# Performance work log

Hardware: AMD Instinct MI355X
Metric: run time of the kernel (lower is better)

Reference implementation:

```python
import jax, jax.numpy as jnp
import numpy as np

N_MELS = 80
HID = 512
N_CLS = 64
DT = 0.1  # LTC integration step (reconstructed DREAMCell constant)


def setup_inputs() -> dict:
    key = jax.random.key(0)
    ks = jax.random.split(key, 16)
    s = lambda fan: 1.0 / np.sqrt(fan)
    inp = {
        "feats": jax.random.normal(ks[0], (32, 2048, N_MELS), dtype=jnp.float32),
        # cell 0: input_dim = N_MELS
        "C0": jax.random.normal(ks[1], (N_MELS, HID), jnp.float32) * s(HID),
        "B0": jax.random.normal(ks[2], (HID, N_MELS), jnp.float32) * s(N_MELS),
        "W0": jax.random.normal(ks[3], (HID, N_MELS), jnp.float32) * s(N_MELS),
        "tau0_0": jnp.float32(1.0),
        "gamma0": jnp.float32(0.25),
        "ltc_tau0": jax.random.normal(ks[4], (HID,), jnp.float32) * 0.1,
        # cell 1: input_dim = HID (receives base_eff of cell 0)
        "C1": jax.random.normal(ks[5], (HID, HID), jnp.float32) * s(HID),
        "B1": jax.random.normal(ks[6], (HID, HID), jnp.float32) * s(HID),
        "W1": jax.random.normal(ks[7], (HID, HID), jnp.float32) * s(HID),
        "tau0_1": jnp.float32(1.0),
        "gamma1": jnp.float32(0.25),
        "ltc_tau1": jax.random.normal(ks[8], (HID,), jnp.float32) * 0.1,
        # head: Linear(2*HID, N_CLS)
        "head_w": jax.random.normal(ks[9], (N_CLS, 2 * HID), jnp.float32) * s(2 * HID),
        "head_b": jnp.zeros((N_CLS,), jnp.float32),
    }
    return inp


def _step_cell(params, h, x_t):
    C, Bm, W, tau0, gamma, ltc_tau = params
    # x_t: (B, D_in), h: (B, HID)
    x_scale = jnp.clip(jnp.linalg.norm(x_t, axis=-1, keepdims=True), 1e-6, None)  # (B,1)
    x_norm = jnp.clip(x_t / x_scale, -1.0, 1.0)
    hd = jax.lax.stop_gradient(h)
    error = x_t - jnp.tanh(hd @ C.T) * x_scale  # (B, D_in)
    rel_err = jnp.minimum(
        jnp.linalg.norm(error, axis=-1) / jax.lax.stop_gradient(x_scale[:, 0]), 4.0
    )  # (B,)
    surprise = jax.nn.sigmoid((rel_err - tau0) / gamma)  # (B,)
    base_eff = x_norm @ Bm.T  # (B, HID)
    err_eff = error @ W.T  # (B, HID)
    input_h = hd * 0.2 + base_eff * 0.6 + err_eff * surprise[:, None] * 0.2
    # LTC update (reconstructed): surprise-modulated liquid time constant
    tau_eff = 1.0 + jax.nn.softplus(ltc_tau)  # (HID,)
    alpha = (DT / tau_eff) * (1.0 + surprise[:, None])
    h_new = h + alpha * (jnp.tanh(input_h) - h)
    return h_new, base_eff


def _forward(feats, cell_params, head_w, head_b):
    B = feats.shape[0]
    h0 = tuple(jnp.zeros((B, HID), feats.dtype) for _ in cell_params)

    def body(hs, x_t):
        x = x_t
        new_hs = []
        for p, h in zip(cell_params, hs):
            h, be = _step_cell(p, h, x)
            new_hs.append(h)
            x = be
        out_t = jnp.concatenate([new_hs[-1], x], axis=-1)  # (B, 2*HID)
        return tuple(new_hs), out_t

    xs = jnp.swapaxes(feats, 0, 1)  # (T, B, N_MELS)
    _, outs = jax.lax.scan(body, h0, xs)  # (T, B, 2*HID)
    outs = jnp.swapaxes(outs, 0, 1)  # (B, T, 2*HID)
    return outs @ head_w.T + head_b  # (B, T, N_CLS)


def reference(feats, C0, B0, W0, tau0_0, gamma0, ltc_tau0,
              C1, B1, W1, tau0_1, gamma1, ltc_tau1, head_w, head_b):
    cell_params = [
        (C0, B0, W0, tau0_0, gamma0, ltc_tau0),
        (C1, B1, W1, tau0_1, gamma1, ltc_tau1),
    ]
    return _forward(feats, cell_params, head_w, head_b)
```

## Files before the change

### kernel.cpp

```cpp
#include <hip/hip_runtime.h>
#include <hip/hip_fp16.h>
#include <math.h>

#define BATCHN 32
#define SEQT   2048
#define NMELS  80
#define HIDN   512
#define NCLSN  64
#define BTROWS (BATCHN*SEQT)

typedef unsigned long long u64;
typedef _Float16 __attribute__((ext_vector_type(2))) h2v;

__device__ inline float wave_sum(float v) {
  #pragma unroll
  for (int o = 32; o > 0; o >>= 1) v += __shfl_xor(v, o, 64);
  return v;
}
__device__ inline float ftanh(float x) {
  float ax = fabsf(x);
  float e = __expf(2.0f*ax);
  float t = 1.0f - 2.0f/(e + 1.0f);
  return copysignf(t, x);
}
__device__ inline unsigned pkh2(float a, float b) {
  __half2 h = __floats2half2_rn(a, b);
  return *(unsigned*)&h;
}
__device__ inline float fdot2(unsigned a, unsigned b, float c) {
#if __has_builtin(__builtin_amdgcn_fdot2)
  union { unsigned u; h2v v; } ua, ub; ua.u = a; ub.u = b;
  return __builtin_amdgcn_fdot2(ua.v, ub.v, c, false);
#else
  union { unsigned u; __half2 h; } ua, ub; ua.u = a; ub.u = b;
  float2 fa = __half22float2(ua.h), fb = __half22float2(ub.h);
  return c + fa.x*fb.x + fa.y*fb.y;
#endif
}
__device__ inline u64 pk64(float v, unsigned ep) {
  union { float f; unsigned u; } c; c.f = v;
  return ((u64)ep << 32) | (u64)c.u;
}
__device__ inline float lo32f(u64 q) {
  union { unsigned u; float f; } c; c.u = (unsigned)q; return c.f;
}
__device__ inline void st64(u64* p, u64 v) {
  __hip_atomic_store(p, v, __ATOMIC_RELAXED, __HIP_MEMORY_SCOPE_AGENT);
}
__device__ inline u64 ld64(const u64* p) {
  return __hip_atomic_load(p, __ATOMIC_RELAXED, __HIP_MEMORY_SCOPE_AGENT);
}

__global__ __launch_bounds__(256) void rownorm_kernel(
    const float* __restrict__ X, float* __restrict__ xs, int M, int K)
{
  int wave = threadIdx.x >> 6, lane = threadIdx.x & 63;
  int m = blockIdx.x*4 + wave;
  if (m >= M) return;
  const float* row = X + (size_t)m*K;
  float acc = 0.f;
  for (int k = lane; k < K; k += 64) { float v = row[k]; acc += v*v; }
  acc = wave_sum(acc);
  if (lane == 0) xs[m] = fmaxf(sqrtf(acc), 1e-6f);
}

__global__ __launch_bounds__(256) void initout_kernel(
    float* __restrict__ out, const float* __restrict__ head_b)
{
  int i4 = blockIdx.x*256 + threadIdx.x;
  float4 v = ((const float4*)head_b)[i4 & 15];
  ((float4*)out)[i4] = v;
}

__global__ __launch_bounds__(256, 1) void recur_kernel(
    const float* __restrict__ feats,
    const float* __restrict__ B0,
    const float* __restrict__ C1, const float* __restrict__ B1,
    const float* __restrict__ W1,
    const float* __restrict__ ltc,
    const float* __restrict__ tau0p, const float* __restrict__ gammap,
    const float* __restrict__ head_w,
    const float* __restrict__ xs0v,
    float* __restrict__ out,
    u64* __restrict__ PG)
{
  const int wg = blockIdx.x;
  const int x = wg & 7, s = (wg >> 3) & 7, qq = wg >> 6;
  const int b = x*4 + qq;
  const int row0 = s*64;
  const int tid = threadIdx.x;
  const int r = tid >> 2, kc = tid & 3;
  const int wid = tid >> 6, lane = tid & 63;

  __shared__ u64      b0t_s[20*512];
  __shared__ float    whh_s[64*68];
  __shared__ float    whb_s[64*68];
  __shared__ unsigned er2_s[256];
  __shared__ unsigned bo2_s[256];
  __shared__ unsigned ft2_s[40];
  __shared__ float    h_s[64];
  __shared__ float    bv_s[64];
  __shared__ float    a0_s[64];
  __shared__ float    red_s[4], red0_s[4];

  unsigned c1a[32], c1b[32];
  unsigned w1h[64];
  unsigned b1h[64];
  {
    const float* srcA = C1 + (size_t)tid*512 + row0;
    const float* srcB = C1 + (size_t)(tid+256)*512 + row0;
    #pragma unroll
    for (int j = 0; j < 16; j++) {
      float4 va = *(const float4*)(srcA + 4*j);
      float4 vb = *(const float4*)(srcB + 4*j);
      c1a[2*j] = pkh2(va.x, va.y); c1a[2*j+1] = pkh2(va.z, va.w);
      c1b[2*j] = pkh2(vb.x, vb.y); c1b[2*j+1] = pkh2(vb.z, vb.w);
    }
  }
  {
    const float* src = W1 + (size_t)(row0 + r)*512 + kc*64;
    #pragma unroll
    for (int u4 = 0; u4 < 16; u4++) {
      float4 va = *(const float4*)(src + 4*u4);
      float4 vb = *(const float4*)(src + 256 + 4*u4);
      w1h[4*u4+0] = pkh2(va.x, vb.x); w1h[4*u4+1] = pkh2(va.y, vb.y);
      w1h[4*u4+2] = pkh2(va.z, vb.z); w1h[4*u4+3] = pkh2(va.w, vb.w);
    }
  }
  {
    const float* src = B1 + (size_t)(row0 + r)*512 + kc*64;
    #pragma unroll
    for (int u4 = 0; u4 < 16; u4++) {
      float4 va = *(const float4*)(src + 4*u4);
      float4 vb = *(const float4*)(src + 256 + 4*u4);
      b1h[4*u4+0] = pkh2(va.x, vb.x); b1h[4*u4+1] = pkh2(va.y, vb.y);
      b1h[4*u4+2] = pkh2(va.z, vb.z); b1h[4*u4+3] = pkh2(va.w, vb.w);
    }
  }
  for (int i = tid; i < 20*512; i += 256) {
    int k4 = i >> 9, row = i & 511;
    float4 v = *(const float4*)(B0 + (size_t)row*80 + 4*k4);
    b0t_s[i] = (u64)pkh2(v.x, v.y) | ((u64)pkh2(v.z, v.w) << 32);
  }
  for (int i = tid; i < 4096; i += 256) {
    int c = i >> 6, j = i & 63;
    whh_s[c*68+j] = head_w[(size_t)c*1024 + row0 + j];
    whb_s[c*68+j] = head_w[(size_t)c*1024 + 512 + row0 + j];
  }
  if (tid < 64) {
    float xv = ltc[row0 + tid];
    float spl = (xv > 20.f) ? xv : log1pf(__expf(xv));
    a0_s[tid] = 0.1f / (1.0f + spl);
    h_s[tid] = 0.f;
  }
  const float tau0v = *tau0p, gmv = *gammap;
  __syncthreads();

  float bev0 = 0.f, bev1 = 0.f, xsc = 1.f, rxs_c = 1.f;
  float ftn = 0.f, rxs0n = 1.f;

  auto shadow = [&]() {
    float fo = __shfl_xor(ftn, 1, 64);
    if (tid < 80 && (tid & 1) == 0) ft2_s[tid >> 1] = pkh2(ftn, fo);
    __syncthreads();
    float a0v = 0.f, a1v = 0.f;
    #pragma unroll
    for (int k4 = 0; k4 < 20; k4++) {
      unsigned fA = ft2_s[2*k4], fB = ft2_s[2*k4+1];
      u64 qa = b0t_s[k4*512 + tid];
      u64 qb = b0t_s[k4*512 + tid + 256];
      a0v = fdot2((unsigned)qa, fA, a0v); a0v = fdot2((unsigned)(qa >> 32), fB, a0v);
      a1v = fdot2((unsigned)qb, fA, a1v); a1v = fdot2((unsigned)(qb >> 32), fB, a1v);
    }
    const float b0n = a0v * rxs0n, b1n = a1v * rxs0n;
    float sq = wave_sum(b0n*b0n + b1n*b1n);
    if (lane == 0) red0_s[wid] = sq;
    __syncthreads();
    const float xsq = red0_s[0]+red0_s[1]+red0_s[2]+red0_s[3];
    const float xs1n = fmaxf(sqrtf(xsq), 1e-6f);
    const float rx1n = 1.0f / xs1n;
    bo2_s[tid] = pkh2(b0n*rx1n, b1n*rx1n);
    __syncthreads();
    float pb = 0.f;
    #pragma unroll
    for (int u4 = 0; u4 < 16; u4++) {
      uint4 ov = *(const uint4*)(bo2_s + kc*64 + 4*u4);
      pb = fdot2(b1h[4*u4+0], ov.x, pb);
      pb = fdot2(b1h[4*u4+1], ov.y, pb);
      pb = fdot2(b1h[4*u4+2], ov.z, pb);
      pb = fdot2(b1h[4*u4+3], ov.w, pb);
    }
    pb += __shfl_xor(pb, 1, 64);
    pb += __shfl_xor(pb, 2, 64);
    if (kc == 0) bv_s[r] = pb;
    bev0 = b0n; bev1 = b1n; xsc = xs1n; rxs_c = rx1n;
  };

  {
    const size_t bt0 = (size_t)b*SEQT;
    if (tid < 80) ftn = feats[bt0*80 + tid];
    rxs0n = 1.0f / xs0v[bt0];
    shadow();
    u64* PGw = PG + ((size_t)0*BATCHN + b)*8*512 + (size_t)s*512;
    st64(&PGw[tid],       pk64(0.f, 1u));
    st64(&PGw[tid + 256], pk64(0.f, 1u));
  }
  {
    const size_t bt1 = (size_t)b*SEQT + 1;
    ftn = (tid < 80) ? feats[bt1*80 + tid] : 0.f;
    rxs0n = 1.0f / xs0v[bt1];
  }
  __syncthreads();

  for (int t = 0; t < SEQT; ++t) {
    const int par = t & 1;
    const unsigned ep = (unsigned)(t + 1);

    const u64* PGr = PG + ((size_t)par*BATCHN + b)*8*512;
    float g0, g1;
    {
      unsigned gg = 0;
      for (;;) {
        bool ok = true;
        float a0 = 0.f, a1 = 0.f;
        #pragma unroll
        for (int s2 = 0; s2 < 8; s2++) {
          u64 q  = ld64(&PGr[s2*512 + tid]);
          u64 q2 = ld64(&PGr[s2*512 + tid + 256]);
          ok &= ((unsigned)(q  >> 32) == ep);
          ok &= ((unsigned)(q2 >> 32) == ep);
          a0 += lo32f(q); a1 += lo32f(q2);
        }
        if (ok || ++gg > (1u<<18)) { g0 = a0; g1 = a1; break; }
      }
    }

    const float e0 = bev0 - xsc*ftanh(g0);
    const float e1 = bev1 - xsc*ftanh(g1);
    er2_s[tid] = pkh2(e0, e1);
    float es = wave_sum(e0*e0 + e1*e1);
    if (lane == 0) red_s[wid] = es;
    __syncthreads();
    const float ess = red_s[0]+red_s[1]+red_s[2]+red_s[3];
    const float rel = fminf(sqrtf(ess)*rxs_c, 4.0f);
    const float sp = 1.0f/(1.0f + __expf(-(rel - tau0v)/gmv));

    float ee = 0.f;
    #pragma unroll
    for (int u4 = 0; u4 < 16; u4++) {
      uint4 ev = *(const uint4*)(er2_s + kc*64 + 4*u4);
      ee = fdot2(w1h[4*u4+0], ev.x, ee);
      ee = fdot2(w1h[4*u4+1], ev.y, ee);
      ee = fdot2(w1h[4*u4+2], ev.z, ee);
      ee = fdot2(w1h[4*u4+3], ev.w, ee);
    }
    ee += __shfl_xor(ee, 1, 64);
    ee += __shfl_xor(ee, 2, 64);
    if (kc == 0) {
      const float hold = h_s[r];
      const float ih = 0.2f*hold + 0.6f*bv_s[r] + 0.2f*sp*ee;
      const float th = ftanh(ih);
      h_s[r] = hold + a0_s[r]*(1.0f + sp)*(th - hold);
    }
    __syncthreads();

    if (t < SEQT-1) {
      float p0 = 0.f, p1 = 0.f;
      #pragma unroll
      for (int j = 0; j < 16; j++) {
        float4 hv = *(const float4*)(h_s + 4*j);
        unsigned hA = pkh2(hv.x, hv.y), hB = pkh2(hv.z, hv.w);
        p0 = fdot2(c1a[2*j],   hA, p0);
        p0 = fdot2(c1a[2*j+1], hB, p0);
        p1 = fdot2(c1b[2*j],   hA, p1);
        p1 = fdot2(c1b[2*j+1], hB, p1);
      }
      u64* PGw = PG + ((size_t)(par^1)*BATCHN + b)*8*512 + (size_t)s*512;
      st64(&PGw[tid],       pk64(p0, ep + 1u));
      st64(&PGw[tid + 256], pk64(p1, ep + 1u));
    }

    {
      const size_t bt = (size_t)b*SEQT + t;
      const int c = r, j0 = kc*16;
      float hacc = 0.f;
      #pragma unroll
      for (int j4 = 0; j4 < 4; j4++) {
        float4 hv4 = *(const float4*)(h_s  + j0 + 4*j4);
        float4 bv4 = *(const float4*)(bv_s + j0 + 4*j4);
        float4 wh  = *(const float4*)(whh_s + c*68 + j0 + 4*j4);
        float4 wb  = *(const float4*)(whb_s + c*68 + j0 + 4*j4);
        hacc += hv4.x*wh.x + hv4.y*wh.y + hv4.z*wh.z + hv4.w*wh.w
              + bv4.x*wb.x + bv4.y*wb.y + bv4.z*wb.z + bv4.w*wb.w;
      }
      hacc += __shfl_xor(hacc, 1, 64);
      hacc += __shfl_xor(hacc, 2, 64);
      if (kc == 0) atomicAdd(&out[bt*64 + c], hacc);
    }
    if (t < SEQT-1) {
      shadow();
      if (t < SEQT-2) {
        const size_t btn = (size_t)b*SEQT + (t+2);
        if (tid < 80) ftn = feats[btn*80 + tid];
        rxs0n = 1.0f / xs0v[btn];
      }
    }
  }
}

extern "C" void kernel_launch(void* const* d_in, const int* in_sizes, int n_in,
                              void* d_out, int out_size, void* d_ws, size_t ws_size,
                              hipStream_t stream)
{
  (void)in_sizes; (void)n_in; (void)out_size;
  const float* feats  = (const float*)d_in[0];
  const float* B0     = (const float*)d_in[2];
  const float* C1     = (const float*)d_in[7];
  const float* B1     = (const float*)d_in[8];
  const float* W1     = (const float*)d_in[9];
  const float* tau0_1 = (const float*)d_in[10];
  const float* gamma1 = (const float*)d_in[11];
  const float* ltc1   = (const float*)d_in[12];
  const float* head_w = (const float*)d_in[13];
  const float* head_b = (const float*)d_in[14];
  float* out = (float*)d_out;

  u64* PG  = (u64*)d_ws;
  float* xs0 = (float*)(PG + (size_t)2*BATCHN*8*HIDN);
  size_t needed = (size_t)((char*)(xs0 + BTROWS) - (char*)d_ws);
  if (ws_size < needed) return;

  rownorm_kernel<<<BTROWS/4, 256, 0, stream>>>(feats, xs0, BTROWS, NMELS);
  initout_kernel<<<(BTROWS*NCLSN/4)/256, 256, 0, stream>>>(out, head_b);
  hipMemsetAsync(PG, 0, (size_t)2*BATCHN*8*HIDN*sizeof(u64), stream);

  void* args[] = { (void*)&feats, (void*)&B0, (void*)&C1, (void*)&B1, (void*)&W1,
                   (void*)&ltc1, (void*)&tau0_1, (void*)&gamma1, (void*)&head_w,
                   (void*)&xs0, (void*)&out, (void*)&PG };
  hipError_t e = hipLaunchCooperativeKernel((void*)recur_kernel, dim3(256), dim3(256),
                                            args, 0, stream);
  if (e != hipSuccess) {
    recur_kernel<<<256, 256, 0, stream>>>(feats, B0, C1, B1, W1, ltc1, tau0_1, gamma1,
                                          head_w, xs0, out, PG);
  }
}
```

Baseline: 10.15 ms.

## Interleave partial-sum exchange layout, swizzle LDS reads, split dot accumulators

Changes the global partial-sum exchange buffer from slice-major to row-major with the 8 slices interleaved, so each reader's 8 polled words sit contiguously in memory. LDS reads of the error and base vectors are rotated per kc lane group to avoid bank conflicts. The 64-bit B0 transpose table is split into two 32-bit arrays, and the dot products use two accumulators each to shorten dependency chains. The interleaved layout makes writers scatter with stride 8, which may hurt store coalescing.

```diff
diff --git a/kernel.cpp b/kernel.cpp
--- a/kernel.cpp
+++ b/kernel.cpp
@@ -92,7 +92,8 @@
   const int r = tid >> 2, kc = tid & 3;
   const int wid = tid >> 6, lane = tid & 63;
 
-  __shared__ u64      b0t_s[20*512];
+  __shared__ unsigned b0lo_s[20*512];
+  __shared__ unsigned b0hi_s[20*512];
   __shared__ float    whh_s[64*68];
   __shared__ float    whb_s[64*68];
   __shared__ unsigned er2_s[256];
@@ -121,8 +122,9 @@
     const float* src = W1 + (size_t)(row0 + r)*512 + kc*64;
     #pragma unroll
     for (int u4 = 0; u4 < 16; u4++) {
-      float4 va = *(const float4*)(src + 4*u4);
-      float4 vb = *(const float4*)(src + 256 + 4*u4);
+      const int f = (u4 + 4*kc) & 15;
+      float4 va = *(const float4*)(src + 4*f);
+      float4 vb = *(const float4*)(src + 256 + 4*f);
       w1h[4*u4+0] = pkh2(va.x, vb.x); w1h[4*u4+1] = pkh2(va.y, vb.y);
       w1h[4*u4+2] = pkh2(va.z, vb.z); w1h[4*u4+3] = pkh2(va.w, vb.w);
     }
@@ -131,8 +133,9 @@
     const float* src = B1 + (size_t)(row0 + r)*512 + kc*64;
     #pragma unroll
     for (int u4 = 0; u4 < 16; u4++) {
-      float4 va = *(const float4*)(src + 4*u4);
-      float4 vb = *(const float4*)(src + 256 + 4*u4);
+      const int f = (u4 + 4*kc) & 15;
+      float4 va = *(const float4*)(src + 4*f);
+      float4 vb = *(const float4*)(src + 256 + 4*f);
       b1h[4*u4+0] = pkh2(va.x, vb.x); b1h[4*u4+1] = pkh2(va.y, vb.y);
       b1h[4*u4+2] = pkh2(va.z, vb.z); b1h[4*u4+3] = pkh2(va.w, vb.w);
     }
@@ -140,7 +143,8 @@
   for (int i = tid; i < 20*512; i += 256) {
     int k4 = i >> 9, row = i & 511;
     float4 v = *(const float4*)(B0 + (size_t)row*80 + 4*k4);
-    b0t_s[i] = (u64)pkh2(v.x, v.y) | ((u64)pkh2(v.z, v.w) << 32);
+    b0lo_s[i] = pkh2(v.x, v.y);
+    b0hi_s[i] = pkh2(v.z, v.w);
   }
   for (int i = tid; i < 4096; i += 256) {
     int c = i >> 6, j = i & 63;
@@ -167,10 +171,10 @@
     #pragma unroll
     for (int k4 = 0; k4 < 20; k4++) {
       unsigned fA = ft2_s[2*k4], fB = ft2_s[2*k4+1];
-      u64 qa = b0t_s[k4*512 + tid];
-      u64 qb = b0t_s[k4*512 + tid + 256];
-      a0v = fdot2((unsigned)qa, fA, a0v); a0v = fdot2((unsigned)(qa >> 32), fB, a0v);
-      a1v = fdot2((unsigned)qb, fA, a1v); a1v = fdot2((unsigned)(qb >> 32), fB, a1v);
+      a0v = fdot2(b0lo_s[k4*512 + tid],       fA, a0v);
+      a0v = fdot2(b0hi_s[k4*512 + tid],       fB, a0v);
+      a1v = fdot2(b0lo_s[k4*512 + tid + 256], fA, a1v);
+      a1v = fdot2(b0hi_s[k4*512 + tid + 256], fB, a1v);
     }
     const float b0n = a0v * rxs0n, b1n = a1v * rxs0n;
     float sq = wave_sum(b0n*b0n + b1n*b1n);
@@ -181,15 +185,17 @@
     const float rx1n = 1.0f / xs1n;
     bo2_s[tid] = pkh2(b0n*rx1n, b1n*rx1n);
     __syncthreads();
-    float pb = 0.f;
+    float pbA = 0.f, pbB = 0.f;
     #pragma unroll
     for (int u4 = 0; u4 < 16; u4++) {
-      uint4 ov = *(const uint4*)(bo2_s + kc*64 + 4*u4);
-      pb = fdot2(b1h[4*u4+0], ov.x, pb);
-      pb = fdot2(b1h[4*u4+1], ov.y, pb);
-      pb = fdot2(b1h[4*u4+2], ov.z, pb);
-      pb = fdot2(b1h[4*u4+3], ov.w, pb);
-    }
+      const int f = (u4 + 4*kc) & 15;
+      uint4 ov = *(const uint4*)(bo2_s + kc*64 + 4*f);
+      pbA = fdot2(b1h[4*u4+0], ov.x, pbA);
+      pbB = fdot2(b1h[4*u4+1], ov.y, pbB);
+      pbA = fdot2(b1h[4*u4+2], ov.z, pbA);
+      pbB = fdot2(b1h[4*u4+3], ov.w, pbB);
+    }
+    float pb = pbA + pbB;
     pb += __shfl_xor(pb, 1, 64);
     pb += __shfl_xor(pb, 2, 64);
     if (kc == 0) bv_s[r] = pb;
@@ -201,9 +207,9 @@
     if (tid < 80) ftn = feats[bt0*80 + tid];
     rxs0n = 1.0f / xs0v[bt0];
     shadow();
-    u64* PGw = PG + ((size_t)0*BATCHN + b)*8*512 + (size_t)s*512;
-    st64(&PGw[tid],       pk64(0.f, 1u));
-    st64(&PGw[tid + 256], pk64(0.f, 1u));
+    u64* PGw = PG + ((size_t)0*BATCHN + b)*4096;
+    st64(&PGw[(size_t)tid*8 + s],       pk64(0.f, 1u));
+    st64(&PGw[(size_t)(tid+256)*8 + s], pk64(0.f, 1u));
   }
   {
     const size_t bt1 = (size_t)b*SEQT + 1;
@@ -216,7 +222,7 @@
     const int par = t & 1;
     const unsigned ep = (unsigned)(t + 1);
 
-    const u64* PGr = PG + ((size_t)par*BATCHN + b)*8*512;
+    const u64* PGr = PG + ((size_t)par*BATCHN + b)*4096;
     float g0, g1;
     {
       unsigned gg = 0;
@@ -225,8 +231,8 @@
         float a0 = 0.f, a1 = 0.f;
         #pragma unroll
         for (int s2 = 0; s2 < 8; s2++) {
-          u64 q  = ld64(&PGr[s2*512 + tid]);
-          u64 q2 = ld64(&PGr[s2*512 + tid + 256]);
+          u64 q  = ld64(&PGr[(size_t)tid*8 + s2]);
+          u64 q2 = ld64(&PGr[(size_t)(tid+256)*8 + s2]);
           ok &= ((unsigned)(q  >> 32) == ep);
           ok &= ((unsigned)(q2 >> 32) == ep);
           a0 += lo32f(q); a1 += lo32f(q2);
@@ -245,15 +251,17 @@
     const float rel = fminf(sqrtf(ess)*rxs_c, 4.0f);
     const float sp = 1.0f/(1.0f + __expf(-(rel - tau0v)/gmv));
 
-    float ee = 0.f;
+    float eeA = 0.f, eeB = 0.f;
     #pragma unroll
     for (int u4 = 0; u4 < 16; u4++) {
-      uint4 ev = *(const uint4*)(er2_s + kc*64 + 4*u4);
-      ee = fdot2(w1h[4*u4+0], ev.x, ee);
-      ee = fdot2(w1h[4*u4+1], ev.y, ee);
-      ee = fdot2(w1h[4*u4+2], ev.z, ee);
-      ee = fdot2(w1h[4*u4+3], ev.w, ee);
-    }
+      const int f = (u4 + 4*kc) & 15;
+      uint4 ev = *(const uint4*)(er2_s + kc*64 + 4*f);
+      eeA = fdot2(w1h[4*u4+0], ev.x, eeA);
+      eeB = fdot2(w1h[4*u4+1], ev.y, eeB);
+      eeA = fdot2(w1h[4*u4+2], ev.z, eeA);
+      eeB = fdot2(w1h[4*u4+3], ev.w, eeB);
+    }
+    float ee = eeA + eeB;
     ee += __shfl_xor(ee, 1, 64);
     ee += __shfl_xor(ee, 2, 64);
     if (kc == 0) {
@@ -265,19 +273,19 @@
     __syncthreads();
 
     if (t < SEQT-1) {
-      float p0 = 0.f, p1 = 0.f;
+      float p0a = 0.f, p0b = 0.f, p1a = 0.f, p1b = 0.f;
       #pragma unroll
       for (int j = 0; j < 16; j++) {
         float4 hv = *(const float4*)(h_s + 4*j);
         unsigned hA = pkh2(hv.x, hv.y), hB = pkh2(hv.z, hv.w);
-        p0 = fdot2(c1a[2*j],   hA, p0);
-        p0 = fdot2(c1a[2*j+1], hB, p0);
-        p1 = fdot2(c1b[2*j],   hA, p1);
-        p1 = fdot2(c1b[2*j+1], hB, p1);
+        p0a = fdot2(c1a[2*j],   hA, p0a);
+        p0b = fdot2(c1a[2*j+1], hB, p0b);
+        p1a = fdot2(c1b[2*j],   hA, p1a);
+        p1b = fdot2(c1b[2*j+1], hB, p1b);
       }
-      u64* PGw = PG + ((size_t)(par^1)*BATCHN + b)*8*512 + (size_t)s*512;
-      st64(&PGw[tid],       pk64(p0, ep + 1u));
-      st64(&PGw[tid + 256], pk64(p1, ep + 1u));
+      u64* PGw = PG + ((size_t)(par^1)*BATCHN + b)*4096;
+      st64(&PGw[(size_t)tid*8 + s],       pk64(p0a + p0b, ep + 1u));
+      st64(&PGw[(size_t)(tid+256)*8 + s], pk64(p1a + p1b, ep + 1u));
     }
 
     {
@@ -326,13 +334,13 @@
   float* out = (float*)d_out;
 
   u64* PG  = (u64*)d_ws;
-  float* xs0 = (float*)(PG + (size_t)2*BATCHN*8*HIDN);
+  float* xs0 = (float*)(PG + (size_t)2*BATCHN*HIDN*8);
   size_t needed = (size_t)((char*)(xs0 + BTROWS) - (char*)d_ws);
   if (ws_size < needed) return;
 
   rownorm_kernel<<<BTROWS/4, 256, 0, stream>>>(feats, xs0, BTROWS, NMELS);
   initout_kernel<<<(BTROWS*NCLSN/4)/256, 256, 0, stream>>>(out, head_b);
-  hipMemsetAsync(PG, 0, (size_t)2*BATCHN*8*HIDN*sizeof(u64), stream);
+  hipMemsetAsync(PG, 0, (size_t)2*BATCHN*HIDN*8*sizeof(u64), stream);
 
   void* args[] = { (void*)&feats, (void*)&B0, (void*)&C1, (void*)&B1, (void*)&W1,
                    (void*)&ltc1, (void*)&tau0_1, (void*)&gamma1, (void*)&head_w,
```

After: 11.69 ms. 15.2% more time.
